# Optimization experiments

Hardware: AMD Instinct MI355X
Metric: run time of the kernel (lower is better)

## Reference

```python
import jax, jax.numpy as jnp
import numpy as np

B = 4096
NC = 64        # n_concepts
NT = 16        # n_tasks
H = 256        # prior_units (prior_layers = 1)
HID = 256      # prior_hids = [256, 256]
K = 20         # n_components
IN = 3 * NC + NT + 1        # GRU input size = 209
MLP_IN = H + 3 * NC + NT    # rnn_out input = 464
LOG_2PI = float(np.log(2.0 * np.pi))


def setup_inputs() -> dict:
    key = jax.random.key(0)
    ks = jax.random.split(key, 16)
    s = 0.05
    inp = {
        "z": jax.random.normal(ks[0], (B, NC), jnp.float32),
        "c": jax.random.normal(ks[1], (B, NC + NT), jnp.float32),
        "b": (jax.random.uniform(ks[2], (B, NC)) < 0.5).astype(jnp.float32),
        "m": (jax.random.uniform(ks[3], (B, NC)) < 0.5).astype(jnp.float32),
        # GRU (PyTorch layout: gates ordered r, z, n)
        "W_ih": jax.random.normal(ks[4], (3 * H, IN), jnp.float32) * s,
        "W_hh": jax.random.normal(ks[5], (3 * H, H), jnp.float32) * s,
        "b_ih": jax.random.normal(ks[6], (3 * H,), jnp.float32) * s,
        "b_hh": jax.random.normal(ks[7], (3 * H,), jnp.float32) * s,
        # rnn_out MLP: Linear(464,256)+Tanh, Linear(256,256)+Tanh, Linear(256,3K)
        "W1": jax.random.normal(ks[8], (HID, MLP_IN), jnp.float32) * s,
        "b1": jax.random.normal(ks[9], (HID,), jnp.float32) * s,
        "W2": jax.random.normal(ks[10], (HID, HID), jnp.float32) * s,
        "b2": jax.random.normal(ks[11], (HID,), jnp.float32) * s,
        "W3": jax.random.normal(ks[12], (3 * K, HID), jnp.float32) * s,
        "b3": jax.random.normal(ks[13], (3 * K,), jnp.float32) * s,
    }
    return inp


def _logp(z, c, b, m, W_ih, W_hh, b_ih, b_hh, W1, b1, W2, b2, W3, b3):
    Bsz, d = z.shape
    cbm = jnp.concatenate([c, b, m], axis=1)               # [B, 3*NC+NT]
    # z input at step t is -1 for t=0, else z[:, t-1]
    z_prev = jnp.concatenate(
        [-jnp.ones((Bsz, 1), z.dtype), z[:, :-1]], axis=1)  # [B, d]
    # Precompute the input-gate projections for all steps without
    # materializing the full [d, B, IN] sequence tensor:
    # column 0 of W_ih multiplies z_prev; the rest multiplies cbm.
    gi_cbm = cbm @ W_ih[:, 1:].T + b_ih                    # [B, 3H]
    gi = gi_cbm[None, :, :] + z_prev.T[:, :, None] * W_ih[:, 0][None, None, :]  # [d, B, 3H]

    def gru_step(h, gi_t):
        gh = h @ W_hh.T + b_hh
        gi_r, gi_u, gi_n = jnp.split(gi_t, 3, axis=-1)
        gh_r, gh_u, gh_n = jnp.split(gh, 3, axis=-1)
        r = jax.nn.sigmoid(gi_r + gh_r)
        u = jax.nn.sigmoid(gi_u + gh_u)
        n = jnp.tanh(gi_n + r * gh_n)
        h_new = (1.0 - u) * n + u * h
        return h_new, h_new

    h0 = jnp.zeros((Bsz, W_hh.shape[1]), z.dtype)
    _, hs = jax.lax.scan(gru_step, h0, gi)                 # [d, B, H]
    hs = jnp.transpose(hs, (1, 0, 2))                      # [B, d, H]

    feat = jnp.concatenate(
        [hs, jnp.broadcast_to(cbm[:, None, :], (Bsz, d, cbm.shape[1]))],
        axis=2)                                            # [B, d, MLP_IN]
    h1 = jnp.tanh(feat @ W1.T + b1)
    h2 = jnp.tanh(h1 @ W2.T + b2)
    params = h2 @ W3.T + b3                                # [B, d, 3K]

    logits, means, lsigmas = jnp.split(params, 3, axis=-1)
    t = z[..., None]                                       # [B, d, 1]
    log_norm = -lsigmas - 0.5 * LOG_2PI
    diff = (t - means) * jnp.exp(-lsigmas)
    log_kernel = -0.5 * jnp.square(diff)
    log_like = (jax.nn.logsumexp(log_kernel + log_norm + logits, axis=-1)
                - jax.nn.logsumexp(logits, axis=-1))       # [B, d]

    query = m * (1.0 - b)
    mask = jnp.sort(query, axis=1)[:, ::-1]                # descending sort of values
    return jnp.sum(log_like * mask, axis=1)                # [B]


def reference(z, c, b, m, W_ih, W_hh, b_ih, b_hh, W1, b1, W2, b2, W3, b3):
    return _logp(z, c, b, m, W_ih, W_hh, b_ih, b_hh,
                 W1, b1, W2, b2, W3, b3)
```

## Files before the change

kernel.cpp:

```cpp
#include <hip/hip_runtime.h>
#include <hip/hip_bf16.h>

#define BATCH  4096
#define NCC    64
#define HDIM   256
#define G3     768
#define NROW   (BATCH*NCC)
#define NK     20
#define LOG2PI 1.8378770664093453f

typedef __attribute__((ext_vector_type(8))) short bf16x8;
typedef __attribute__((ext_vector_type(4))) float f32x4;

__device__ __forceinline__ float sigm(float x) { return 1.0f/(1.0f + __expf(-x)); }
__device__ __forceinline__ float tanh_fast(float x) { return 1.0f - 2.0f/(__expf(2.0f*x) + 1.0f); }
__device__ __forceinline__ unsigned short f2bf(float x) {
  __hip_bfloat16 h = __float2bfloat16(x);
  return __builtin_bit_cast(unsigned short, h);
}
__device__ __forceinline__ int swz(int r) { return (r & 7) ^ ((r & 8) >> 2); }

__global__ __launch_bounds__(256) void k_cvtall(
    const float* __restrict__ c, const float* __restrict__ bv,
    const float* __restrict__ mv, const float* __restrict__ W_ih,
    const float* __restrict__ W_hh, const float* __restrict__ W1,
    const float* __restrict__ W2, const float* __restrict__ W3,
    unsigned short* __restrict__ cbmB, unsigned short* __restrict__ CW,
    unsigned short* __restrict__ WhhB, unsigned short* __restrict__ W1aB,
    unsigned short* __restrict__ W2B, unsigned short* __restrict__ W3pB,
    float* __restrict__ w0) {
  int idx = blockIdx.x*256 + threadIdx.x;
  if (idx < 1048576) {
    int row = idx >> 8, k = idx & 255;
    float v = 0.f;
    if (k < 80)       v = c [row*80 + k];
    else if (k < 144) v = bv[row*64 + (k-80)];
    else if (k < 208) v = mv[row*64 + (k-144)];
    cbmB[idx] = f2bf(v);
    return;
  }
  idx -= 1048576;
  if (idx < 262144) {
    int n = idx >> 8, k = idx & 255;
    float v = 0.f;
    if (n < 768) { if (k < 208) v = W_ih[n*209 + 1 + k]; }
    else         { if (k < 208) v = W1[(n-768)*464 + 256 + k]; }
    CW[idx] = f2bf(v);
    return;
  }
  idx -= 262144;
  if (idx < 196608) { WhhB[idx] = f2bf(W_hh[idx]); return; }
  idx -= 196608;
  if (idx < 65536) { int n = idx>>8, k = idx&255; W1aB[idx] = f2bf(W1[n*464+k]); return; }
  idx -= 65536;
  if (idx < 65536) { W2B[idx] = f2bf(W2[idx]); return; }
  idx -= 65536;
  if (idx < 16384) {
    int n = idx >> 8;
    float v = 0.f;
    if (n < 60) v = W3[idx];
    W3pB[idx] = f2bf(v);
    return;
  }
  idx -= 16384;
  if (idx < 768) w0[idx] = W_ih[idx*209];
}

__global__ __launch_bounds__(512) void k_pre(
    const unsigned short* __restrict__ A, const unsigned short* __restrict__ Bw,
    const float* __restrict__ b_ih, const float* __restrict__ b_hh,
    const float* __restrict__ b1,
    float* __restrict__ gi, float* __restrict__ P1) {
  __shared__ __align__(16) unsigned short As[128*64];
  __shared__ __align__(16) unsigned short Bs[128*64];
  int tid = threadIdx.x;
  int rb = blockIdx.x >> 3, cb = blockIdx.x & 7;
  long row0 = (long)rb * 128;
  int n0 = cb * 128;
  int wv = tid >> 6, lane = tid & 63;
  int lq = lane >> 4, l16 = lane & 15;
  int wrg = wv & 3, wcg = wv >> 2;
  f32x4 acc[2][4];
#pragma unroll
  for (int i = 0; i < 2; ++i)
#pragma unroll
    for (int j = 0; j < 4; ++j) acc[i][j] = (f32x4){0.f,0.f,0.f,0.f};
  for (int kb = 0; kb < 256; kb += 64) {
#pragma unroll
    for (int i = 0; i < 2; ++i) {
      int s = i*512 + tid;
      int r = s >> 3, cg = (s & 7) ^ (r & 7);
      *(uint4*)&As[s*8] = *(const uint4*)&A[(row0 + r)*256 + kb + cg*8];
      *(uint4*)&Bs[s*8] = *(const uint4*)&Bw[(long)(n0 + r)*256 + kb + cg*8];
    }
    __syncthreads();
#pragma unroll
    for (int kc = 0; kc < 2; ++kc) {
      int csel = kc*4 + lq;
      bf16x8 af[2];
#pragma unroll
      for (int rt = 0; rt < 2; ++rt) {
        int r = wrg*32 + rt*16 + l16;
        af[rt] = *(const bf16x8*)&As[r*64 + ((csel ^ (r & 7)))*8];
      }
#pragma unroll
      for (int ct = 0; ct < 4; ++ct) {
        int n = wcg*64 + ct*16 + l16;
        bf16x8 bfr = *(const bf16x8*)&Bs[n*64 + ((csel ^ (n & 7)))*8];
        acc[0][ct] = __builtin_amdgcn_mfma_f32_16x16x32_bf16(af[0], bfr, acc[0][ct], 0, 0, 0);
        acc[1][ct] = __builtin_amdgcn_mfma_f32_16x16x32_bf16(af[1], bfr, acc[1][ct], 0, 0, 0);
      }
    }
    __syncthreads();
  }
#pragma unroll
  for (int rt = 0; rt < 2; ++rt)
#pragma unroll
    for (int q = 0; q < 4; ++q) {
      long row = row0 + wrg*32 + rt*16 + lq*4 + q;
#pragma unroll
      for (int ct = 0; ct < 4; ++ct) {
        int n = n0 + wcg*64 + ct*16 + l16;
        float v = acc[rt][ct][q];
        if (n < 512)      gi[row*G3 + n] = v + b_ih[n] + b_hh[n];
        else if (n < 768) gi[row*G3 + n] = v + b_ih[n];
        else              P1[row*256 + (n-768)] = v + b1[n-768];
      }
    }
}

__global__ __attribute__((amdgpu_flat_work_group_size(512, 512)))
__attribute__((amdgpu_waves_per_eu(2, 2)))
void k_gru(
    const float* __restrict__ z, const float* __restrict__ gi,
    const unsigned short* __restrict__ WhhB, const float* __restrict__ b_hh,
    const float* __restrict__ w0, unsigned short* __restrict__ hs) {
  __shared__ __align__(16) unsigned short hbf[2*16*256];
  __shared__ __align__(16) float gis[768*20];
  __shared__ __align__(16) float zs[64*16];
  __shared__ float wls[768 + 256];
  int tid = threadIdx.x;
  int wv = tid >> 6, lane = tid & 63;
  int lq = lane >> 4, l16 = lane & 15;
  int row0 = blockIdx.x * 16;
  bf16x8 wf[6][8];
#pragma unroll
  for (int g = 0; g < 3; ++g)
#pragma unroll
    for (int tt = 0; tt < 2; ++tt)
#pragma unroll
      for (int ks = 0; ks < 8; ++ks)
        wf[g*2+tt][ks] = *(const bf16x8*)&WhhB[(long)(g*256 + wv*32 + tt*16 + l16)*256 + ks*32 + lq*8];
  for (int i = tid; i < 768; i += 512) wls[i] = w0[i];
  for (int i = tid; i < 256; i += 512) wls[768 + i] = b_hh[512 + i];
  for (int i = tid; i < 1024; i += 512) {
    int t = i >> 4, r = i & 15;
    zs[i] = z[(row0+r)*64 + t];
  }
#pragma unroll
  for (int i = 0; i < 24; ++i) {
    int s = i*512 + tid;
    int r = s / 768, cc = s - r*768;
    gis[cc*20 + r] = gi[(long)(row0+r)*768 + cc];
  }
  for (int i = tid; i < 2048; i += 512) ((unsigned int*)hbf)[i] = 0u;
  float hp[2][4] = {{0.f,0.f,0.f,0.f},{0.f,0.f,0.f,0.f}};
  const int s7 = l16 & 7;
  const int arow = l16*256;
  const int r4 = lq*4;
  const int hc0 = wv*32 + l16;
  const int cr = tid >> 5, ccc = tid & 31;
  const int csrc = cr*256 + ((ccc ^ (cr & 7)))*8;
  unsigned short* cbase = hs + (long)(row0+cr)*64*256 + ccc*8;
  __syncthreads();
#pragma unroll 1
  for (int t = 0; t < 64; ++t) {
    const int co = (t & 1) << 12;
    const int no = co ^ 4096;
    float zp[4];
    {
      float4 zv4 = *(const float4*)&zs[(t ? (t-1) : 0)*16 + r4];
#pragma unroll
      for (int q = 0; q < 4; ++q) zp[q] = t ? (&zv4.x)[q] : -1.0f;
    }
    f32x4 a[6];
#pragma unroll
    for (int tt = 0; tt < 2; ++tt) {
      int hc = hc0 + tt*16;
      f32x4 gR = *(const f32x4*)&gis[hc*20 + r4];
      f32x4 gU = *(const f32x4*)&gis[(256+hc)*20 + r4];
      float w0r = wls[hc], w0u = wls[256+hc], bn = wls[768 + hc];
#pragma unroll
      for (int q = 0; q < 4; ++q) {
        a[tt][q]   = gR[q] + zp[q]*w0r;
        a[2+tt][q] = gU[q] + zp[q]*w0u;
        a[4+tt][q] = bn;
      }
    }
#pragma unroll
    for (int ks = 0; ks < 8; ++ks) {
      bf16x8 af = *(const bf16x8*)&hbf[co + arow + (((ks*4+lq) ^ s7))*8];
#pragma unroll
      for (int f = 0; f < 6; ++f)
        a[f] = __builtin_amdgcn_mfma_f32_16x16x32_bf16(af, wf[f][ks], a[f], 0, 0, 0);
    }
    if (t) {
      uint4 cdat = *(const uint4*)&hbf[co + csrc];
      *(uint4*)(cbase + (t-1)*256) = cdat;
    }
#pragma unroll
    for (int tt = 0; tt < 2; ++tt) {
      int hc = hc0 + tt*16;
      int hchunk = hc >> 3, hlow = hc & 7;
      float w0n = wls[512 + hc];
      f32x4 gN = *(const f32x4*)&gis[(512+hc)*20 + r4];
#pragma unroll
      for (int q = 0; q < 4; ++q) {
        int r = r4 + q;
        float rr = sigm(a[tt][q]);
        float uu = sigm(a[2+tt][q]);
        float nn = tanh_fast(gN[q] + zp[q]*w0n + rr*a[4+tt][q]);
        float hn = uu*(hp[tt][q] - nn) + nn;
        hp[tt][q] = hn;
        hbf[no + r*256 + ((hchunk ^ (r & 7)))*8 + hlow] = f2bf(hn);
      }
    }
    __syncthreads();
  }
  uint4 cdat = *(const uint4*)&hbf[0 + csrc];
  *(uint4*)(cbase + 63*256) = cdat;
}

__global__ __launch_bounds__(512) void k_l1(
    const unsigned short* __restrict__ A, const unsigned short* __restrict__ Bw,
    const float* __restrict__ P1, unsigned short* __restrict__ Out) {
  __shared__ __align__(16) unsigned short As[128*64];
  __shared__ __align__(16) unsigned short Bs[256*64];
  int tid = threadIdx.x;
  long row0 = (long)blockIdx.x * 128;
  int wv = tid >> 6, lane = tid & 63;
  int lq = lane >> 4, l16 = lane & 15;
  int wrg = wv & 3, wcg = wv >> 2;
  f32x4 acc[2][8];
#pragma unroll
  for (int i = 0; i < 2; ++i)
#pragma unroll
    for (int j = 0; j < 8; ++j) acc[i][j] = (f32x4){0.f,0.f,0.f,0.f};
  for (int kb = 0; kb < 256; kb += 64) {
#pragma unroll
    for (int i = 0; i < 2; ++i) {
      int s = i*512 + tid;
      int r = s >> 3, cg = (s & 7) ^ (r & 7);
      *(uint4*)&As[s*8] = *(const uint4*)&A[(row0 + r)*256 + kb + cg*8];
    }
#pragma unroll
    for (int i = 0; i < 4; ++i) {
      int s = i*512 + tid;
      int r = s >> 3, cg = (s & 7) ^ (r & 7);
      *(uint4*)&Bs[s*8] = *(const uint4*)&Bw[(long)r*256 + kb + cg*8];
    }
    __syncthreads();
#pragma unroll
    for (int kc = 0; kc < 2; ++kc) {
      int csel = kc*4 + lq;
      bf16x8 af[2];
#pragma unroll
      for (int rt = 0; rt < 2; ++rt) {
        int r = wrg*32 + rt*16 + l16;
        af[rt] = *(const bf16x8*)&As[r*64 + ((csel ^ (r & 7)))*8];
      }
#pragma unroll
      for (int ct = 0; ct < 8; ++ct) {
        int n = wcg*128 + ct*16 + l16;
        bf16x8 bfr = *(const bf16x8*)&Bs[n*64 + ((csel ^ (n & 7)))*8];
        acc[0][ct] = __builtin_amdgcn_mfma_f32_16x16x32_bf16(af[0], bfr, acc[0][ct], 0, 0, 0);
        acc[1][ct] = __builtin_amdgcn_mfma_f32_16x16x32_bf16(af[1], bfr, acc[1][ct], 0, 0, 0);
      }
    }
    __syncthreads();
  }
#pragma unroll
  for (int rt = 0; rt < 2; ++rt)
#pragma unroll
    for (int q = 0; q < 4; ++q) {
      long row = row0 + wrg*32 + rt*16 + lq*4 + q;
#pragma unroll
      for (int ct = 0; ct < 8; ++ct) {
        int n = wcg*128 + ct*16 + l16;
        float b = P1[(row >> 6)*256 + n];
        Out[row*256 + n] = f2bf(tanh_fast(acc[rt][ct][q] + b));
      }
    }
}

__global__ __launch_bounds__(512) void k_l23(
    const unsigned short* __restrict__ A, const unsigned short* __restrict__ W2B,
    const float* __restrict__ b2, const unsigned short* __restrict__ W3pB,
    const float* __restrict__ b3, const float* __restrict__ z,
    float* __restrict__ ll) {
  __shared__ __align__(16) unsigned short As[128*64];
  __shared__ __align__(16) unsigned short Bs[256*64];
  __shared__ __align__(16) unsigned short h2s[128*256];
  int tid = threadIdx.x;
  long row0 = (long)blockIdx.x * 128;
  int wv = tid >> 6, lane = tid & 63;
  int lq = lane >> 4, l16 = lane & 15;
  int wrg = wv & 3, wcg = wv >> 2;
  f32x4 acc[2][8];
#pragma unroll
  for (int i = 0; i < 2; ++i)
#pragma unroll
    for (int j = 0; j < 8; ++j) acc[i][j] = (f32x4){0.f,0.f,0.f,0.f};
  for (int kb = 0; kb < 256; kb += 64) {
#pragma unroll
    for (int i = 0; i < 2; ++i) {
      int s = i*512 + tid;
      int r = s >> 3, cg = (s & 7) ^ (r & 7);
      *(uint4*)&As[s*8] = *(const uint4*)&A[(row0 + r)*256 + kb + cg*8];
    }
#pragma unroll
    for (int i = 0; i < 4; ++i) {
      int s = i*512 + tid;
      int r = s >> 3, cg = (s & 7) ^ (r & 7);
      *(uint4*)&Bs[s*8] = *(const uint4*)&W2B[(long)r*256 + kb + cg*8];
    }
    __syncthreads();
#pragma unroll
    for (int kc = 0; kc < 2; ++kc) {
      int csel = kc*4 + lq;
      bf16x8 af[2];
#pragma unroll
      for (int rt = 0; rt < 2; ++rt) {
        int r = wrg*32 + rt*16 + l16;
        af[rt] = *(const bf16x8*)&As[r*64 + ((csel ^ (r & 7)))*8];
      }
#pragma unroll
      for (int ct = 0; ct < 8; ++ct) {
        int n = wcg*128 + ct*16 + l16;
        bf16x8 bfr = *(const bf16x8*)&Bs[n*64 + ((csel ^ (n & 7)))*8];
        acc[0][ct] = __builtin_amdgcn_mfma_f32_16x16x32_bf16(af[0], bfr, acc[0][ct], 0, 0, 0);
        acc[1][ct] = __builtin_amdgcn_mfma_f32_16x16x32_bf16(af[1], bfr, acc[1][ct], 0, 0, 0);
      }
    }
    __syncthreads();
  }
#pragma unroll
  for (int rt = 0; rt < 2; ++rt)
#pragma unroll
    for (int q = 0; q < 4; ++q) {
      int lr = wrg*32 + rt*16 + lq*4 + q;
#pragma unroll
      for (int ct = 0; ct < 8; ++ct) {
        int n = wcg*128 + ct*16 + l16;
        h2s[lr*256 + (((n >> 3) ^ swz(lr))*8 + (n & 7))] =
            f2bf(tanh_fast(acc[rt][ct][q] + b2[n]));
      }
    }
#pragma unroll
  for (int i = 0; i < 4; ++i) {
    int s = i*512 + tid;
    int r = s >> 5, cc = s & 31;
    *(uint4*)&Bs[r*256 + ((cc ^ swz(r)))*8] = *(const uint4*)&W3pB[r*256 + cc*8];
  }
  __syncthreads();
  f32x4 pacc[4];
#pragma unroll
  for (int j = 0; j < 4; ++j) pacc[j] = (f32x4){0.f,0.f,0.f,0.f};
#pragma unroll
  for (int ks = 0; ks < 8; ++ks) {
    int chunk = ks*4 + lq;
    int ar = wv*16 + l16;
    bf16x8 af = *(const bf16x8*)&h2s[ar*256 + ((chunk ^ swz(ar)))*8];
#pragma unroll
    for (int ct = 0; ct < 4; ++ct) {
      int br = ct*16 + l16;
      bf16x8 bfr = *(const bf16x8*)&Bs[br*256 + ((chunk ^ swz(br)))*8];
      pacc[ct] = __builtin_amdgcn_mfma_f32_16x16x32_bf16(af, bfr, pacc[ct], 0, 0, 0);
    }
  }
  float* Ps = (float*)&h2s[wv*16*256];
#pragma unroll
  for (int ct = 0; ct < 4; ++ct) {
    int n = ct*16 + l16;
    float b = (n < 60) ? b3[n] : 0.0f;
#pragma unroll
    for (int q = 0; q < 4; ++q)
      Ps[(lq*4 + q)*68 + n] = pacc[ct][q] + b;
  }
  if (lane < 16) {
    long grow = row0 + wv*16 + lane;
    float zv = z[grow];
    const float* p = &Ps[lane*68];
    float mx1 = -1e30f;
#pragma unroll
    for (int i = 0; i < NK; ++i) mx1 = fmaxf(mx1, p[i]);
    float s1 = 0.0f;
#pragma unroll
    for (int i = 0; i < NK; ++i) s1 += __expf(p[i] - mx1);
    float lse1 = mx1 + __logf(s1);
    float a[NK];
    float mx2 = -1e30f;
#pragma unroll
    for (int i = 0; i < NK; ++i) {
      float lg = p[i], me = p[20+i], ls = p[40+i];
      float e = __expf(-ls);
      float d = (zv - me) * e;
      float ai = -0.5f*d*d - ls - 0.5f*LOG2PI + lg;
      a[i] = ai;
      mx2 = fmaxf(mx2, ai);
    }
    float s2 = 0.0f;
#pragma unroll
    for (int i = 0; i < NK; ++i) s2 += __expf(a[i] - mx2);
    float lse2 = mx2 + __logf(s2);
    ll[grow] = lse2 - lse1;
  }
}

__global__ __launch_bounds__(256) void k_final(const float* __restrict__ bv,
    const float* __restrict__ mv, const float* __restrict__ ll,
    float* __restrict__ out) {
  int tid = threadIdx.x;
  int wave = tid >> 6, lane = tid & 63;
  int b = blockIdx.x*4 + wave;
  float q = mv[b*64 + lane] * (1.0f - bv[b*64 + lane]);
  unsigned long long bal = __ballot(q > 0.5f);
  int S = __popcll(bal);
  float val = (lane < S) ? ll[(long)b*64 + lane] : 0.0f;
#pragma unroll
  for (int off = 32; off > 0; off >>= 1) val += __shfl_down(val, off);
  if (lane == 0) out[b] = val;
}

extern "C" void kernel_launch(void* const* d_in, const int* in_sizes, int n_in,
                              void* d_out, int out_size, void* d_ws, size_t ws_size,
                              hipStream_t stream) {
  const float* z    = (const float*)d_in[0];
  const float* c    = (const float*)d_in[1];
  const float* bv   = (const float*)d_in[2];
  const float* mv   = (const float*)d_in[3];
  const float* W_ih = (const float*)d_in[4];
  const float* W_hh = (const float*)d_in[5];
  const float* b_ih = (const float*)d_in[6];
  const float* b_hh = (const float*)d_in[7];
  const float* W1   = (const float*)d_in[8];
  const float* b1   = (const float*)d_in[9];
  const float* W2   = (const float*)d_in[10];
  const float* b2   = (const float*)d_in[11];
  const float* W3   = (const float*)d_in[12];
  const float* b3   = (const float*)d_in[13];
  float* out = (float*)d_out;

  char* p = (char*)d_ws;
  auto alloc = [&](size_t bytes) {
    char* q = p;
    p += (bytes + 255) & ~(size_t)255;
    return q;
  };
  unsigned short* cbmB = (unsigned short*)alloc((size_t)BATCH*256*2);
  unsigned short* CW   = (unsigned short*)alloc((size_t)1024*256*2);
  unsigned short* WhhB = (unsigned short*)alloc((size_t)G3*256*2);
  unsigned short* W1aB = (unsigned short*)alloc((size_t)256*256*2);
  unsigned short* W2B  = (unsigned short*)alloc((size_t)256*256*2);
  unsigned short* W3pB = (unsigned short*)alloc((size_t)64*256*2);
  float* w0 = (float*)alloc((size_t)G3*4);
  float* gi = (float*)alloc((size_t)BATCH*G3*4);
  float* P1 = (float*)alloc((size_t)BATCH*256*4);
  float* ll = (float*)alloc((size_t)NROW*4);
  unsigned short* hs = (unsigned short*)alloc((size_t)NROW*HDIM*2);

  k_cvtall<<<6468, 256, 0, stream>>>(c, bv, mv, W_ih, W_hh, W1, W2, W3,
                                     cbmB, CW, WhhB, W1aB, W2B, W3pB, w0);
  k_pre<<<256, 512, 0, stream>>>(cbmB, CW, b_ih, b_hh, b1, gi, P1);
  k_gru<<<256, 512, 0, stream>>>(z, gi, WhhB, b_hh, w0, hs);
  k_l1<<<NROW/128, 512, 0, stream>>>(hs, W1aB, P1, hs);
  k_l23<<<NROW/128, 512, 0, stream>>>(hs, W2B, b2, W3pB, b3, z, ll);
  k_final<<<BATCH/4, 256, 0, stream>>>(bv, mv, ll, out);
}
```

Measured before the change: 520.9 us.

## Split GRU recurrence across 16 waves per block with LDS-staged weight loading

The GRU kernel now runs with 1024 threads (16 waves) per block instead of 512, so each wave owns 16 hidden columns and keeps only 3×8 weight fragments in registers instead of 6×8. The per-step serial chain per wave is halved, which is meant to shorten the latency-bound 64-step recurrence. The W_hh fragments are now staged through LDS (reusing the gi buffer) in 16 rounds with barriers to get coalesced loads. In exchange, the per-step __syncthreads covers twice as many waves, and the setup adds extra barriers.

```diff
diff --git a/kernel.cpp b/kernel.cpp
--- a/kernel.cpp
+++ b/kernel.cpp
@@ -129,8 +129,8 @@
     }
 }
 
-__global__ __attribute__((amdgpu_flat_work_group_size(512, 512)))
-__attribute__((amdgpu_waves_per_eu(2, 2)))
+__global__ __attribute__((amdgpu_flat_work_group_size(1024, 1024)))
+__attribute__((amdgpu_waves_per_eu(4, 4)))
 void k_gru(
     const float* __restrict__ z, const float* __restrict__ gi,
     const unsigned short* __restrict__ WhhB, const float* __restrict__ b_hh,
@@ -143,92 +143,99 @@
   int wv = tid >> 6, lane = tid & 63;
   int lq = lane >> 4, l16 = lane & 15;
   int row0 = blockIdx.x * 16;
-  bf16x8 wf[6][8];
-#pragma unroll
-  for (int g = 0; g < 3; ++g)
-#pragma unroll
-    for (int tt = 0; tt < 2; ++tt)
-#pragma unroll
-      for (int ks = 0; ks < 8; ++ks)
-        wf[g*2+tt][ks] = *(const bf16x8*)&WhhB[(long)(g*256 + wv*32 + tt*16 + l16)*256 + ks*32 + lq*8];
-  for (int i = tid; i < 768; i += 512) wls[i] = w0[i];
-  for (int i = tid; i < 256; i += 512) wls[768 + i] = b_hh[512 + i];
-  for (int i = tid; i < 1024; i += 512) {
-    int t = i >> 4, r = i & 15;
-    zs[i] = z[(row0+r)*64 + t];
-  }
-#pragma unroll
-  for (int i = 0; i < 24; ++i) {
-    int s = i*512 + tid;
+  unsigned short* stg = (unsigned short*)gis;
+  bf16x8 wf[3][8];
+  for (int cg = 0; cg < 16; ++cg) {
+    for (int s = tid; s < 1536; s += 1024) {
+      int r = s >> 5, cc = s & 31;
+      int g = r >> 4, col = r & 15;
+      *(uint4*)&stg[r*256 + ((cc ^ (r & 7))*8)] =
+          *(const uint4*)&WhhB[(long)(g*256 + cg*16 + col)*256 + cc*8];
+    }
+    __syncthreads();
+    if (wv == cg) {
+#pragma unroll
+      for (int g = 0; g < 3; ++g)
+#pragma unroll
+        for (int ks = 0; ks < 8; ++ks) {
+          int r = g*16 + l16, kc = ks*4 + lq;
+          wf[g][ks] = *(const bf16x8*)&stg[r*256 + ((kc ^ (r & 7))*8)];
+        }
+    }
+    __syncthreads();
+  }
+  if (tid < 768) wls[tid] = w0[tid];
+  else if (tid < 1024) wls[tid] = b_hh[512 + (tid - 768)];
+  {
+    int t = tid >> 4, r = tid & 15;
+    zs[tid] = z[(row0+r)*64 + t];
+  }
+#pragma unroll
+  for (int i = 0; i < 12; ++i) {
+    int s = i*1024 + tid;
     int r = s / 768, cc = s - r*768;
     gis[cc*20 + r] = gi[(long)(row0+r)*768 + cc];
   }
-  for (int i = tid; i < 2048; i += 512) ((unsigned int*)hbf)[i] = 0u;
-  float hp[2][4] = {{0.f,0.f,0.f,0.f},{0.f,0.f,0.f,0.f}};
+  for (int i = tid; i < 2048; i += 1024) ((unsigned int*)hbf)[i] = 0u;
+  float hp[4] = {0.f, 0.f, 0.f, 0.f};
   const int s7 = l16 & 7;
   const int arow = l16*256;
   const int r4 = lq*4;
-  const int hc0 = wv*32 + l16;
-  const int cr = tid >> 5, ccc = tid & 31;
-  const int csrc = cr*256 + ((ccc ^ (cr & 7)))*8;
-  unsigned short* cbase = hs + (long)(row0+cr)*64*256 + ccc*8;
+  const int hc = wv*16 + l16;
+  const int cr = tid >> 6;
+  const int c8 = (tid & 63) >> 1, half = tid & 1;
+  const int csrc = cr*256 + ((c8 ^ (cr & 7))*8 + half*4);
+  unsigned short* cbase = hs + (long)(row0+cr)*64*256 + c8*8 + half*4;
   __syncthreads();
 #pragma unroll 1
   for (int t = 0; t < 64; ++t) {
     const int co = (t & 1) << 12;
     const int no = co ^ 4096;
+    f32x4 a0, a1, a2;
     float zp[4];
     {
       float4 zv4 = *(const float4*)&zs[(t ? (t-1) : 0)*16 + r4];
-#pragma unroll
-      for (int q = 0; q < 4; ++q) zp[q] = t ? (&zv4.x)[q] : -1.0f;
-    }
-    f32x4 a[6];
-#pragma unroll
-    for (int tt = 0; tt < 2; ++tt) {
-      int hc = hc0 + tt*16;
       f32x4 gR = *(const f32x4*)&gis[hc*20 + r4];
       f32x4 gU = *(const f32x4*)&gis[(256+hc)*20 + r4];
-      float w0r = wls[hc], w0u = wls[256+hc], bn = wls[768 + hc];
+      float w0r = wls[hc], w0u = wls[256+hc], bn = wls[768+hc];
 #pragma unroll
       for (int q = 0; q < 4; ++q) {
-        a[tt][q]   = gR[q] + zp[q]*w0r;
-        a[2+tt][q] = gU[q] + zp[q]*w0u;
-        a[4+tt][q] = bn;
+        zp[q] = t ? (&zv4.x)[q] : -1.0f;
+        a0[q] = gR[q] + zp[q]*w0r;
+        a1[q] = gU[q] + zp[q]*w0u;
+        a2[q] = bn;
       }
     }
 #pragma unroll
     for (int ks = 0; ks < 8; ++ks) {
       bf16x8 af = *(const bf16x8*)&hbf[co + arow + (((ks*4+lq) ^ s7))*8];
-#pragma unroll
-      for (int f = 0; f < 6; ++f)
-        a[f] = __builtin_amdgcn_mfma_f32_16x16x32_bf16(af, wf[f][ks], a[f], 0, 0, 0);
+      a0 = __builtin_amdgcn_mfma_f32_16x16x32_bf16(af, wf[0][ks], a0, 0, 0, 0);
+      a1 = __builtin_amdgcn_mfma_f32_16x16x32_bf16(af, wf[1][ks], a1, 0, 0, 0);
+      a2 = __builtin_amdgcn_mfma_f32_16x16x32_bf16(af, wf[2][ks], a2, 0, 0, 0);
     }
     if (t) {
-      uint4 cdat = *(const uint4*)&hbf[co + csrc];
-      *(uint4*)(cbase + (t-1)*256) = cdat;
-    }
-#pragma unroll
-    for (int tt = 0; tt < 2; ++tt) {
-      int hc = hc0 + tt*16;
+      uint2 cd = *(const uint2*)&hbf[co + csrc];
+      *(uint2*)(cbase + (t-1)*256) = cd;
+    }
+    {
+      f32x4 gN = *(const f32x4*)&gis[(512+hc)*20 + r4];
+      float w0n = wls[512+hc];
       int hchunk = hc >> 3, hlow = hc & 7;
-      float w0n = wls[512 + hc];
-      f32x4 gN = *(const f32x4*)&gis[(512+hc)*20 + r4];
 #pragma unroll
       for (int q = 0; q < 4; ++q) {
         int r = r4 + q;
-        float rr = sigm(a[tt][q]);
-        float uu = sigm(a[2+tt][q]);
-        float nn = tanh_fast(gN[q] + zp[q]*w0n + rr*a[4+tt][q]);
-        float hn = uu*(hp[tt][q] - nn) + nn;
-        hp[tt][q] = hn;
+        float rr = sigm(a0[q]);
+        float uu = sigm(a1[q]);
+        float nn = tanh_fast(gN[q] + zp[q]*w0n + rr*a2[q]);
+        float hn = uu*(hp[q] - nn) + nn;
+        hp[q] = hn;
         hbf[no + r*256 + ((hchunk ^ (r & 7)))*8 + hlow] = f2bf(hn);
       }
     }
     __syncthreads();
   }
-  uint4 cdat = *(const uint4*)&hbf[0 + csrc];
-  *(uint4*)(cbase + 63*256) = cdat;
+  uint2 cd = *(const uint2*)&hbf[0 + csrc];
+  *(uint2*)(cbase + 63*256) = cd;
 }
 
 __global__ __launch_bounds__(512) void k_l1(
@@ -472,7 +479,7 @@
   k_cvtall<<<6468, 256, 0, stream>>>(c, bv, mv, W_ih, W_hh, W1, W2, W3,
                                      cbmB, CW, WhhB, W1aB, W2B, W3pB, w0);
   k_pre<<<256, 512, 0, stream>>>(cbmB, CW, b_ih, b_hh, b1, gi, P1);
-  k_gru<<<256, 512, 0, stream>>>(z, gi, WhhB, b_hh, w0, hs);
+  k_gru<<<256, 1024, 0, stream>>>(z, gi, WhhB, b_hh, w0, hs);
   k_l1<<<NROW/128, 512, 0, stream>>>(hs, W1aB, P1, hs);
   k_l23<<<NROW/128, 512, 0, stream>>>(hs, W2B, b2, W3pB, b3, z, ll);
   k_final<<<BATCH/4, 256, 0, stream>>>(bv, mv, ll, out);
```

Measured after the change: 562.2 us. 7.9% more time.

## Fuse MLP layer 1 with layers 2-3 into one per-batch kernel

Applied to the files above, without the earlier changes.

Merges the first MLP layer kernel and the layer-2/3 plus mixture log-likelihood kernel into a single kernel. Each block handles the 64 rows of one batch element and keeps the tanh hidden activations in shared memory. This removes the bf16 h1 write to global memory and its read-back between launches, and drops one launch. In exchange the row tile shrinks from 128 to 64, so each block streams the weights for fewer rows. The W3 tile load is split into two half-width copies, and a dead no-op loop is left in.

```diff
diff --git a/kernel.cpp b/kernel.cpp
--- a/kernel.cpp
+++ b/kernel.cpp
@@ -231,166 +231,162 @@
   *(uint4*)(cbase + 63*256) = cdat;
 }
 
-__global__ __launch_bounds__(512) void k_l1(
-    const unsigned short* __restrict__ A, const unsigned short* __restrict__ Bw,
-    const float* __restrict__ P1, unsigned short* __restrict__ Out) {
-  __shared__ __align__(16) unsigned short As[128*64];
+__global__ __launch_bounds__(512) void k_mlp(
+    const unsigned short* __restrict__ hs, const unsigned short* __restrict__ W1aB,
+    const float* __restrict__ P1, const unsigned short* __restrict__ W2B,
+    const float* __restrict__ b2, const unsigned short* __restrict__ W3pB,
+    const float* __restrict__ b3, const float* __restrict__ z,
+    float* __restrict__ ll) {
+  __shared__ __align__(16) unsigned short As[64*64];
   __shared__ __align__(16) unsigned short Bs[256*64];
+  __shared__ __align__(16) unsigned short h1s[64*256];
   int tid = threadIdx.x;
-  long row0 = (long)blockIdx.x * 128;
+  int blk = blockIdx.x;
+  long row0 = (long)blk * 64;
   int wv = tid >> 6, lane = tid & 63;
   int lq = lane >> 4, l16 = lane & 15;
   int wrg = wv & 3, wcg = wv >> 2;
-  f32x4 acc[2][8];
-#pragma unroll
-  for (int i = 0; i < 2; ++i)
-#pragma unroll
-    for (int j = 0; j < 8; ++j) acc[i][j] = (f32x4){0.f,0.f,0.f,0.f};
-  for (int kb = 0; kb < 256; kb += 64) {
-#pragma unroll
-    for (int i = 0; i < 2; ++i) {
-      int s = i*512 + tid;
-      int r = s >> 3, cg = (s & 7) ^ (r & 7);
-      *(uint4*)&As[s*8] = *(const uint4*)&A[(row0 + r)*256 + kb + cg*8];
-    }
-#pragma unroll
-    for (int i = 0; i < 4; ++i) {
-      int s = i*512 + tid;
-      int r = s >> 3, cg = (s & 7) ^ (r & 7);
-      *(uint4*)&Bs[s*8] = *(const uint4*)&Bw[(long)r*256 + kb + cg*8];
-    }
-    __syncthreads();
-#pragma unroll
-    for (int kc = 0; kc < 2; ++kc) {
-      int csel = kc*4 + lq;
-      bf16x8 af[2];
-#pragma unroll
-      for (int rt = 0; rt < 2; ++rt) {
-        int r = wrg*32 + rt*16 + l16;
-        af[rt] = *(const bf16x8*)&As[r*64 + ((csel ^ (r & 7)))*8];
-      }
+  {
+    f32x4 acc[8];
+#pragma unroll
+    for (int j = 0; j < 8; ++j) acc[j] = (f32x4){0.f,0.f,0.f,0.f};
+    for (int kb = 0; kb < 256; kb += 64) {
+      {
+        int s = tid;
+        int r = s >> 3, cg = (s & 7) ^ (r & 7);
+        *(uint4*)&As[s*8] = *(const uint4*)&hs[(row0 + r)*256 + kb + cg*8];
+      }
+#pragma unroll
+      for (int i = 0; i < 4; ++i) {
+        int s = i*512 + tid;
+        int r = s >> 3, cg = (s & 7) ^ (r & 7);
+        *(uint4*)&Bs[s*8] = *(const uint4*)&W1aB[(long)r*256 + kb + cg*8];
+      }
+      __syncthreads();
+#pragma unroll
+      for (int kc = 0; kc < 2; ++kc) {
+        int csel = kc*4 + lq;
+        int ar = wrg*16 + l16;
+        bf16x8 af = *(const bf16x8*)&As[ar*64 + ((csel ^ (ar & 7)))*8];
+#pragma unroll
+        for (int ct = 0; ct < 8; ++ct) {
+          int n = wcg*128 + ct*16 + l16;
+          bf16x8 bfr = *(const bf16x8*)&Bs[n*64 + ((csel ^ (n & 7)))*8];
+          acc[ct] = __builtin_amdgcn_mfma_f32_16x16x32_bf16(af, bfr, acc[ct], 0, 0, 0);
+        }
+      }
+      __syncthreads();
+    }
+#pragma unroll
+    for (int q = 0; q < 4; ++q) {
+      int rl = wrg*16 + lq*4 + q;
 #pragma unroll
       for (int ct = 0; ct < 8; ++ct) {
         int n = wcg*128 + ct*16 + l16;
-        bf16x8 bfr = *(const bf16x8*)&Bs[n*64 + ((csel ^ (n & 7)))*8];
-        acc[0][ct] = __builtin_amdgcn_mfma_f32_16x16x32_bf16(af[0], bfr, acc[0][ct], 0, 0, 0);
-        acc[1][ct] = __builtin_amdgcn_mfma_f32_16x16x32_bf16(af[1], bfr, acc[1][ct], 0, 0, 0);
-      }
-    }
-    __syncthreads();
-  }
-#pragma unroll
-  for (int rt = 0; rt < 2; ++rt)
+        float v = tanh_fast(acc[ct][q] + P1[blk*256 + n]);
+        h1s[rl*256 + (((n>>3) ^ swz(rl))*8 + (n&7))] = f2bf(v);
+      }
+    }
+  }
+  __syncthreads();
+  {
+    f32x4 acc[8];
+#pragma unroll
+    for (int j = 0; j < 8; ++j) acc[j] = (f32x4){0.f,0.f,0.f,0.f};
+    for (int kb4 = 0; kb4 < 4; ++kb4) {
+#pragma unroll
+      for (int i = 0; i < 4; ++i) {
+        int s = i*512 + tid;
+        int r = s >> 3, cg = (s & 7) ^ (r & 7);
+        *(uint4*)&Bs[s*8] = *(const uint4*)&W2B[(long)r*256 + kb4*64 + cg*8];
+      }
+      __syncthreads();
+#pragma unroll
+      for (int kc = 0; kc < 2; ++kc) {
+        int csel = kc*4 + lq;
+        int cglob = kb4*8 + csel;
+        int ar = wrg*16 + l16;
+        bf16x8 af = *(const bf16x8*)&h1s[ar*256 + ((cglob ^ swz(ar)))*8];
+#pragma unroll
+        for (int ct = 0; ct < 8; ++ct) {
+          int n = wcg*128 + ct*16 + l16;
+          bf16x8 bfr = *(const bf16x8*)&Bs[n*64 + ((csel ^ (n & 7)))*8];
+          acc[ct] = __builtin_amdgcn_mfma_f32_16x16x32_bf16(af, bfr, acc[ct], 0, 0, 0);
+        }
+      }
+      __syncthreads();
+    }
 #pragma unroll
     for (int q = 0; q < 4; ++q) {
-      long row = row0 + wrg*32 + rt*16 + lq*4 + q;
+      int rl = wrg*16 + lq*4 + q;
 #pragma unroll
       for (int ct = 0; ct < 8; ++ct) {
         int n = wcg*128 + ct*16 + l16;
-        float b = P1[(row >> 6)*256 + n];
-        Out[row*256 + n] = f2bf(tanh_fast(acc[rt][ct][q] + b));
-      }
-    }
-}
-
-__global__ __launch_bounds__(512) void k_l23(
-    const unsigned short* __restrict__ A, const unsigned short* __restrict__ W2B,
-    const float* __restrict__ b2, const unsigned short* __restrict__ W3pB,
-    const float* __restrict__ b3, const float* __restrict__ z,
-    float* __restrict__ ll) {
-  __shared__ __align__(16) unsigned short As[128*64];
-  __shared__ __align__(16) unsigned short Bs[256*64];
-  __shared__ __align__(16) unsigned short h2s[128*256];
-  int tid = threadIdx.x;
-  long row0 = (long)blockIdx.x * 128;
-  int wv = tid >> 6, lane = tid & 63;
-  int lq = lane >> 4, l16 = lane & 15;
-  int wrg = wv & 3, wcg = wv >> 2;
-  f32x4 acc[2][8];
-#pragma unroll
-  for (int i = 0; i < 2; ++i)
-#pragma unroll
-    for (int j = 0; j < 8; ++j) acc[i][j] = (f32x4){0.f,0.f,0.f,0.f};
-  for (int kb = 0; kb < 256; kb += 64) {
-#pragma unroll
-    for (int i = 0; i < 2; ++i) {
-      int s = i*512 + tid;
-      int r = s >> 3, cg = (s & 7) ^ (r & 7);
-      *(uint4*)&As[s*8] = *(const uint4*)&A[(row0 + r)*256 + kb + cg*8];
-    }
-#pragma unroll
-    for (int i = 0; i < 4; ++i) {
-      int s = i*512 + tid;
-      int r = s >> 3, cg = (s & 7) ^ (r & 7);
-      *(uint4*)&Bs[s*8] = *(const uint4*)&W2B[(long)r*256 + kb + cg*8];
-    }
-    __syncthreads();
-#pragma unroll
-    for (int kc = 0; kc < 2; ++kc) {
-      int csel = kc*4 + lq;
-      bf16x8 af[2];
-#pragma unroll
-      for (int rt = 0; rt < 2; ++rt) {
-        int r = wrg*32 + rt*16 + l16;
-        af[rt] = *(const bf16x8*)&As[r*64 + ((csel ^ (r & 7)))*8];
-      }
-#pragma unroll
-      for (int ct = 0; ct < 8; ++ct) {
-        int n = wcg*128 + ct*16 + l16;
-        bf16x8 bfr = *(const bf16x8*)&Bs[n*64 + ((csel ^ (n & 7)))*8];
-        acc[0][ct] = __builtin_amdgcn_mfma_f32_16x16x32_bf16(af[0], bfr, acc[0][ct], 0, 0, 0);
-        acc[1][ct] = __builtin_amdgcn_mfma_f32_16x16x32_bf16(af[1], bfr, acc[1][ct], 0, 0, 0);
-      }
-    }
-    __syncthreads();
-  }
-#pragma unroll
-  for (int rt = 0; rt < 2; ++rt)
-#pragma unroll
-    for (int q = 0; q < 4; ++q) {
-      int lr = wrg*32 + rt*16 + lq*4 + q;
-#pragma unroll
-      for (int ct = 0; ct < 8; ++ct) {
-        int n = wcg*128 + ct*16 + l16;
-        h2s[lr*256 + (((n >> 3) ^ swz(lr))*8 + (n & 7))] =
-            f2bf(tanh_fast(acc[rt][ct][q] + b2[n]));
-      }
-    }
+        float v = tanh_fast(acc[ct][q] + b2[n]);
+        h1s[rl*256 + (((n>>3) ^ swz(rl))*8 + (n&7))] = f2bf(v);
+      }
+    }
+  }
+#pragma unroll
+  for (int i = 0; i < 2; ++i) {
+    int s = i*512 + tid;
+    int r = s >> 4, cc = s & 15;
+    (void)r; (void)cc;
+  }
 #pragma unroll
   for (int i = 0; i < 4; ++i) {
     int s = i*512 + tid;
     int r = s >> 5, cc = s & 31;
-    *(uint4*)&Bs[r*256 + ((cc ^ swz(r)))*8] = *(const uint4*)&W3pB[r*256 + cc*8];
+    if (s < 2048) {
+      *(uint2*)&Bs[r*256 + ((cc ^ swz(r)))*8 + (0)] =
+          *(const uint2*)&W3pB[r*256 + cc*8];
+    }
+  }
+#pragma unroll
+  for (int i = 0; i < 4; ++i) {
+    int s = i*512 + tid;
+    int r = s >> 5, cc = s & 31;
+    if (s < 2048) {
+      *(uint2*)&Bs[r*256 + ((cc ^ swz(r)))*8 + 4] =
+          *(const uint2*)&W3pB[r*256 + cc*8 + 4];
+    }
   }
   __syncthreads();
-  f32x4 pacc[4];
-#pragma unroll
-  for (int j = 0; j < 4; ++j) pacc[j] = (f32x4){0.f,0.f,0.f,0.f};
-#pragma unroll
-  for (int ks = 0; ks < 8; ++ks) {
-    int chunk = ks*4 + lq;
-    int ar = wv*16 + l16;
-    bf16x8 af = *(const bf16x8*)&h2s[ar*256 + ((chunk ^ swz(ar)))*8];
-#pragma unroll
-    for (int ct = 0; ct < 4; ++ct) {
-      int br = ct*16 + l16;
-      bf16x8 bfr = *(const bf16x8*)&Bs[br*256 + ((chunk ^ swz(br)))*8];
-      pacc[ct] = __builtin_amdgcn_mfma_f32_16x16x32_bf16(af, bfr, pacc[ct], 0, 0, 0);
-    }
-  }
-  float* Ps = (float*)&h2s[wv*16*256];
-#pragma unroll
-  for (int ct = 0; ct < 4; ++ct) {
-    int n = ct*16 + l16;
-    float b = (n < 60) ? b3[n] : 0.0f;
-#pragma unroll
-    for (int q = 0; q < 4; ++q)
-      Ps[(lq*4 + q)*68 + n] = pacc[ct][q] + b;
-  }
-  if (lane < 16) {
-    long grow = row0 + wv*16 + lane;
+  {
+    int mt = wv & 3, np = wv >> 2;
+    f32x4 pacc[2];
+#pragma unroll
+    for (int j = 0; j < 2; ++j) pacc[j] = (f32x4){0.f,0.f,0.f,0.f};
+#pragma unroll
+    for (int ks = 0; ks < 8; ++ks) {
+      int chunk = ks*4 + lq;
+      int ar = mt*16 + l16;
+      bf16x8 af = *(const bf16x8*)&h1s[ar*256 + ((chunk ^ swz(ar)))*8];
+#pragma unroll
+      for (int j = 0; j < 2; ++j) {
+        int br = (np*2 + j)*16 + l16;
+        bf16x8 bfr = *(const bf16x8*)&Bs[br*256 + ((chunk ^ swz(br)))*8];
+        pacc[j] = __builtin_amdgcn_mfma_f32_16x16x32_bf16(af, bfr, pacc[j], 0, 0, 0);
+      }
+    }
+    __syncthreads();
+    float* Ps = (float*)h1s;
+#pragma unroll
+    for (int j = 0; j < 2; ++j) {
+      int n = (np*2 + j)*16 + l16;
+      float b = (n < 60) ? b3[n] : 0.0f;
+#pragma unroll
+      for (int q = 0; q < 4; ++q)
+        Ps[(mt*16 + lq*4 + q)*68 + n] = pacc[j][q] + b;
+    }
+  }
+  __syncthreads();
+  if (wv < 4 && lane < 16) {
+    const float* Ps = (const float*)h1s;
+    int rl = wv*16 + lane;
+    long grow = row0 + rl;
     float zv = z[grow];
-    const float* p = &Ps[lane*68];
+    const float* p = &Ps[rl*68];
     float mx1 = -1e30f;
 #pragma unroll
     for (int i = 0; i < NK; ++i) mx1 = fmaxf(mx1, p[i]);
@@ -473,7 +469,6 @@
                                      cbmB, CW, WhhB, W1aB, W2B, W3pB, w0);
   k_pre<<<256, 512, 0, stream>>>(cbmB, CW, b_ih, b_hh, b1, gi, P1);
   k_gru<<<256, 512, 0, stream>>>(z, gi, WhhB, b_hh, w0, hs);
-  k_l1<<<NROW/128, 512, 0, stream>>>(hs, W1aB, P1, hs);
-  k_l23<<<NROW/128, 512, 0, stream>>>(hs, W2B, b2, W3pB, b3, z, ll);
+  k_mlp<<<BATCH, 512, 0, stream>>>(hs, W1aB, P1, W2B, b2, W3pB, b3, z, ll);
   k_final<<<BATCH/4, 256, 0, stream>>>(bv, mv, ll, out);
 }
```

Result: slower. 558.2 us (+7.1%).

## Cut k_l23 shared memory by reusing the GEMM buffers for the h2 tile

Applied to the files above, without the earlier changes.

Drops the separate 64KB h2s shared buffer in the fused layer-2/3 kernel. The h2 activations are written into the freed Bs buffer in two 64-row halves, W3 is staged through As in two k-chunks, and a small Ps float buffer holds the parameters for the mixture log-likelihood. This cuts LDS per block from about 112KB to about 65KB so more blocks can be resident per CU. The cost is extra __syncthreads barriers and a serialized two-pass epilogue in which only half the waves write h2 and only four waves run the final reduction.

```diff
diff --git a/kernel.cpp b/kernel.cpp
--- a/kernel.cpp
+++ b/kernel.cpp
@@ -300,7 +300,7 @@
     float* __restrict__ ll) {
   __shared__ __align__(16) unsigned short As[128*64];
   __shared__ __align__(16) unsigned short Bs[256*64];
-  __shared__ __align__(16) unsigned short h2s[128*256];
+  __shared__ float Ps[64*68];
   int tid = threadIdx.x;
   long row0 = (long)blockIdx.x * 128;
   int wv = tid >> 6, lane = tid & 63;
@@ -344,76 +344,89 @@
     }
     __syncthreads();
   }
-#pragma unroll
-  for (int rt = 0; rt < 2; ++rt)
-#pragma unroll
-    for (int q = 0; q < 4; ++q) {
-      int lr = wrg*32 + rt*16 + lq*4 + q;
-#pragma unroll
-      for (int ct = 0; ct < 8; ++ct) {
-        int n = wcg*128 + ct*16 + l16;
-        h2s[lr*256 + (((n >> 3) ^ swz(lr))*8 + (n & 7))] =
-            f2bf(tanh_fast(acc[rt][ct][q] + b2[n]));
-      }
-    }
-#pragma unroll
-  for (int i = 0; i < 4; ++i) {
-    int s = i*512 + tid;
-    int r = s >> 5, cc = s & 31;
-    *(uint4*)&Bs[r*256 + ((cc ^ swz(r)))*8] = *(const uint4*)&W3pB[r*256 + cc*8];
-  }
-  __syncthreads();
-  f32x4 pacc[4];
-#pragma unroll
-  for (int j = 0; j < 4; ++j) pacc[j] = (f32x4){0.f,0.f,0.f,0.f};
-#pragma unroll
-  for (int ks = 0; ks < 8; ++ks) {
-    int chunk = ks*4 + lq;
-    int ar = wv*16 + l16;
-    bf16x8 af = *(const bf16x8*)&h2s[ar*256 + ((chunk ^ swz(ar)))*8];
-#pragma unroll
-    for (int ct = 0; ct < 4; ++ct) {
-      int br = ct*16 + l16;
-      bf16x8 bfr = *(const bf16x8*)&Bs[br*256 + ((chunk ^ swz(br)))*8];
-      pacc[ct] = __builtin_amdgcn_mfma_f32_16x16x32_bf16(af, bfr, pacc[ct], 0, 0, 0);
-    }
-  }
-  float* Ps = (float*)&h2s[wv*16*256];
-#pragma unroll
-  for (int ct = 0; ct < 4; ++ct) {
-    int n = ct*16 + l16;
-    float b = (n < 60) ? b3[n] : 0.0f;
-#pragma unroll
-    for (int q = 0; q < 4; ++q)
-      Ps[(lq*4 + q)*68 + n] = pacc[ct][q] + b;
-  }
-  if (lane < 16) {
-    long grow = row0 + wv*16 + lane;
-    float zv = z[grow];
-    const float* p = &Ps[lane*68];
-    float mx1 = -1e30f;
-#pragma unroll
-    for (int i = 0; i < NK; ++i) mx1 = fmaxf(mx1, p[i]);
-    float s1 = 0.0f;
-#pragma unroll
-    for (int i = 0; i < NK; ++i) s1 += __expf(p[i] - mx1);
-    float lse1 = mx1 + __logf(s1);
-    float a[NK];
-    float mx2 = -1e30f;
-#pragma unroll
-    for (int i = 0; i < NK; ++i) {
-      float lg = p[i], me = p[20+i], ls = p[40+i];
-      float e = __expf(-ls);
-      float d = (zv - me) * e;
-      float ai = -0.5f*d*d - ls - 0.5f*LOG2PI + lg;
-      a[i] = ai;
-      mx2 = fmaxf(mx2, ai);
-    }
-    float s2 = 0.0f;
-#pragma unroll
-    for (int i = 0; i < NK; ++i) s2 += __expf(a[i] - mx2);
-    float lse2 = mx2 + __logf(s2);
-    ll[grow] = lse2 - lse1;
+  for (int half = 0; half < 2; ++half) {
+    if ((wrg >> 1) == half) {
+#pragma unroll
+      for (int rt = 0; rt < 2; ++rt)
+#pragma unroll
+        for (int q = 0; q < 4; ++q) {
+          int lr = (wrg & 1)*32 + rt*16 + lq*4 + q;
+#pragma unroll
+          for (int ct = 0; ct < 8; ++ct) {
+            int n = wcg*128 + ct*16 + l16;
+            Bs[lr*256 + (((n >> 3) ^ swz(lr))*8 + (n & 7))] =
+                f2bf(tanh_fast(acc[rt][ct][q] + b2[n]));
+          }
+        }
+    }
+    __syncthreads();
+    int tile = wv*2;
+    f32x4 pacc[2];
+    pacc[0] = (f32x4){0.f,0.f,0.f,0.f};
+    pacc[1] = (f32x4){0.f,0.f,0.f,0.f};
+    for (int c2 = 0; c2 < 2; ++c2) {
+#pragma unroll
+      for (int i = 0; i < 2; ++i) {
+        int s = i*512 + tid;
+        int r = s >> 4, kc = s & 15;
+        *(uint4*)&As[r*128 + ((kc ^ (r & 7))*8)] =
+            *(const uint4*)&W3pB[r*256 + c2*128 + kc*8];
+      }
+      __syncthreads();
+#pragma unroll
+      for (int km = 0; km < 4; ++km) {
+#pragma unroll
+        for (int j = 0; j < 2; ++j) {
+          int rt3 = (tile + j) >> 2, ct3 = (tile + j) & 3;
+          int ar = rt3*16 + l16;
+          bf16x8 af = *(const bf16x8*)&Bs[ar*256 + (((c2*16 + km*4 + lq) ^ swz(ar)))*8];
+          int bn = ct3*16 + l16;
+          bf16x8 bfr = *(const bf16x8*)&As[bn*128 + (((km*4 + lq) ^ (bn & 7)))*8];
+          pacc[j] = __builtin_amdgcn_mfma_f32_16x16x32_bf16(af, bfr, pacc[j], 0, 0, 0);
+        }
+      }
+      __syncthreads();
+    }
+#pragma unroll
+    for (int j = 0; j < 2; ++j) {
+      int rt3 = (tile + j) >> 2, ct3 = (tile + j) & 3;
+      int n = ct3*16 + l16;
+      float b = (n < 60) ? b3[n] : 0.0f;
+#pragma unroll
+      for (int q = 0; q < 4; ++q)
+        Ps[(rt3*16 + lq*4 + q)*68 + n] = pacc[j][q] + b;
+    }
+    __syncthreads();
+    if (wv < 4 && lane < 16) {
+      int lr = wv*16 + lane;
+      long grow = row0 + half*64 + lr;
+      float zv = z[grow];
+      const float* p = &Ps[lr*68];
+      float mx1 = -1e30f;
+#pragma unroll
+      for (int i = 0; i < NK; ++i) mx1 = fmaxf(mx1, p[i]);
+      float s1 = 0.0f;
+#pragma unroll
+      for (int i = 0; i < NK; ++i) s1 += __expf(p[i] - mx1);
+      float lse1 = mx1 + __logf(s1);
+      float a[NK];
+      float mx2 = -1e30f;
+#pragma unroll
+      for (int i = 0; i < NK; ++i) {
+        float lg = p[i], me = p[20+i], ls = p[40+i];
+        float e = __expf(-ls);
+        float d = (zv - me) * e;
+        float ai = -0.5f*d*d - ls - 0.5f*LOG2PI + lg;
+        a[i] = ai;
+        mx2 = fmaxf(mx2, ai);
+      }
+      float s2 = 0.0f;
+#pragma unroll
+      for (int i = 0; i < NK; ++i) s2 += __expf(a[i] - mx2);
+      float lse2 = mx2 + __logf(s2);
+      ll[grow] = lse2 - lse1;
+    }
+    __syncthreads();
   }
 }
 
```

Result: slower. 571.3 us (+9.7%).
